# Performance work log

Hardware: AMD Instinct MI355X
Metric: run time of the kernel (lower is better)

The kernel has to match this reference:

```python
import jax, jax.numpy as jnp
import numpy as np

B, N, DIM, H, DH = 8, 1024, 512, 8, 64
INNER = H * DH  # 512
G = DH // 4     # SE(3) groups of size 4 per head


def setup_inputs() -> dict:
    key = jax.random.key(0)
    ks = jax.random.split(key, 6)
    x = jax.random.normal(ks[0], (B, N, DIM), jnp.float32)
    rotations = jax.random.normal(ks[1], (B, N, 3, 3), jnp.float32)
    translations = jax.random.normal(ks[2], (B, N, 3), jnp.float32)
    # JaxLinear init: trunc-normal std = 1/sqrt(fan_in), zero bias
    w_qkv = jax.random.normal(ks[3], (DIM, 3 * INNER), jnp.float32) * (1.0 / np.sqrt(DIM))
    b_qkv = jnp.zeros((3 * INNER,), jnp.float32)
    w_out = jax.random.normal(ks[4], (INNER, DIM), jnp.float32) * (1.0 / np.sqrt(INNER))
    b_out = jnp.zeros((DIM,), jnp.float32)
    return {"x": x, "rotations": rotations, "translations": translations,
            "w_qkv": w_qkv, "b_qkv": b_qkv, "w_out": w_out, "b_out": b_out}


def _apply_pose(P, t, transpose):
    # P: [B,N,4,4]; t: [B,H,N,DH] -> reshape to groups of 4 and rotate each group
    tg = t.reshape(B, H, N, G, 4)
    sub = 'bnji,bhncj->bhnci' if transpose else 'bnij,bhncj->bhnci'
    return jnp.einsum(sub, P, tg).reshape(B, H, N, DH)


def reference(x, rotations, translations, w_qkv, b_qkv, w_out, b_out):
    scale = DH ** -0.5
    qkv = x @ w_qkv + b_qkv                      # [B,N,3*INNER]
    q, k, v = jnp.split(qkv, 3, axis=-1)
    to_heads = lambda t: t.reshape(B, N, H, DH).transpose(0, 2, 1, 3)  # b n (h d) -> b h n d
    q, k, v = to_heads(q), to_heads(k), to_heads(v)

    # SE(3) pose matrices
    eye4 = jnp.eye(4, dtype=x.dtype)
    Rt = jnp.swapaxes(rotations, -1, -2)
    t_inv = -jnp.einsum('bnij,bnj->bni', Rt, translations)
    P_qinv = (jnp.broadcast_to(eye4, (B, N, 4, 4))
              .at[..., :3, :3].set(Rt)
              .at[..., :3, 3].set(t_inv))       # inverted query poses
    P_kv = (jnp.broadcast_to(eye4, (B, N, 4, 4))
            .at[..., :3, :3].set(rotations)
            .at[..., :3, 3].set(translations))  # key/value poses

    # per-token rotation of q/k/v (q uses P_qinv^T per original einsum)
    q = _apply_pose(P_qinv, q, transpose=True)
    k = _apply_pose(P_kv, k, transpose=False)
    v = _apply_pose(P_kv, v, transpose=False)   # v_transform=True

    attn = jax.nn.softmax(jnp.einsum('bhqd,bhkd->bhqk', q, k) * scale, axis=-1)
    out = jnp.einsum('bhqk,bhkd->bhqd', attn, v)
    out = _apply_pose(P_qinv, out, transpose=False)  # inverse transform on output

    out = out.transpose(0, 2, 1, 3).reshape(B, N, INNER)  # b h n d -> b n (h d)
    return out @ w_out + b_out
```

## Files before the change

kernel.cpp:

```cpp
#include <hip/hip_runtime.h>
#include <math.h>

#define BSZ   8
#define NSEQ  1024
#define DIM   512
#define NH    8
#define DH    64
#define INNER 512
#define NTOK  (BSZ*NSEQ)
#define QKVN  (3*INNER)

typedef __bf16 bf16x8 __attribute__((ext_vector_type(8)));
typedef float  f32x4  __attribute__((ext_vector_type(4)));

#define QSCL (0.125f * 1.44269504088896f)

static __device__ __forceinline__ ushort f2bf(float f) {
    union { float f; unsigned u; } v; v.f = f;
    unsigned r = (v.u + 0x7FFFu + ((v.u >> 16) & 1u)) >> 16;
    return (ushort)r;
}
static __device__ __forceinline__ float bf2f(ushort u) {
    union { unsigned u; float f; } v; v.u = ((unsigned)u) << 16;
    return v.f;
}
static __device__ __forceinline__ void split2(float x, ushort& h, ushort& l) {
    h = f2bf(x);
    l = f2bf(x - bf2f(h));
}
static __device__ __forceinline__ void async16(const void* g, void* l) {
    __builtin_amdgcn_global_load_lds(
        (const __attribute__((address_space(1))) unsigned int*)g,
        (__attribute__((address_space(3))) unsigned int*)l, 16, 0, 0);
}

__global__ __launch_bounds__(256) void split_cvt_kernel(
    const float* __restrict__ in, ushort* __restrict__ oh, ushort* __restrict__ ol)
{
    const int i = blockIdx.x * 256 + threadIdx.x;
    float4 v = ((const float4*)in)[i];
    ushort4 h, l;
    split2(v.x, h.x, l.x); split2(v.y, h.y, l.y);
    split2(v.z, h.z, l.z); split2(v.w, h.w, l.w);
    ((ushort4*)oh)[i] = h;
    ((ushort4*)ol)[i] = l;
}

__global__ __launch_bounds__(256) void tconv_kernel(
    const float* __restrict__ in, ushort* __restrict__ outh, int K, int F)
{
    __shared__ float tile[32][33];
    const int bx = blockIdx.x;
    const int by = blockIdx.y;
    const int lx = threadIdx.x & 31, ly = threadIdx.x >> 5;
#pragma unroll
    for (int u = 0; u < 4; u++) {
        const int k = by*32 + ly + u*8;
        tile[ly + u*8][lx] = in[(size_t)k*F + bx*32 + lx];
    }
    __syncthreads();
#pragma unroll
    for (int u = 0; u < 4; u++) {
        const int f = bx*32 + ly + u*8;
        outh[(size_t)f*K + by*32 + lx] = f2bf(tile[lx][ly + u*8]);
    }
}

__global__ __launch_bounds__(256) void qkv_gemm_split(
    const ushort* __restrict__ Agh, const ushort* __restrict__ Bgh,
    const ushort* __restrict__ Bgl,
    const float* __restrict__ bias, const float* __restrict__ rot,
    const float* __restrict__ trans,
    ushort* __restrict__ qb, ushort* __restrict__ kb, ushort* __restrict__ vt)
{
    extern __shared__ __align__(16) char smem[];

    const int tid  = threadIdx.x;
    const int lane = tid & 63;
    const int w    = tid >> 6;
    const int c    = lane & 15;
    const int quad = lane >> 4;
    const int wr   = w >> 1, wc = w & 1;
    const int tn   = blockIdx.x;
    const int tf   = blockIdx.y;

    f32x4 acc[4][4] = {};

    const ushort* wp = (w == 0) ? Agh : (w == 1) ? Bgh : Bgl;
    const ushort* wbase = wp + (size_t)((w == 0 ? tf : tn)*128 + c)*DIM + quad*8;
    const int lbase = w * 8192;

    auto stage = [&](int k0, int buf) {
        if (w < 3) {
#pragma unroll
            for (int g = 0; g < 8; g++)
                async16(wbase + (size_t)g*16*DIM + k0,
                        smem + buf*24576 + lbase + g*1024);
        }
    };

    stage(0, 0);

    for (int ch = 0; ch < 16; ch++) {
        const int cur = ch & 1, nxt = cur ^ 1;
        if (ch < 15) {
            stage((ch+1)*32, nxt);
            __asm__ volatile("s_waitcnt vmcnt(8)\n\ts_barrier" ::: "memory");
        } else {
            __asm__ volatile("s_waitcnt vmcnt(0)\n\ts_barrier" ::: "memory");
        }

        const char* B = smem + cur*24576;
        bf16x8 fa[4], fbh[4], fbl[4];
#pragma unroll
        for (int i = 0; i < 4; i++)
            fa[i] = *(const bf16x8*)(B + (wr*4 + i)*1024 + lane*16);
#pragma unroll
        for (int j = 0; j < 4; j++) {
            fbh[j] = *(const bf16x8*)(B +  8192 + (wc*4 + j)*1024 + lane*16);
            fbl[j] = *(const bf16x8*)(B + 16384 + (wc*4 + j)*1024 + lane*16);
        }
#pragma unroll
        for (int i = 0; i < 4; i++)
#pragma unroll
            for (int j = 0; j < 4; j++) {
                acc[i][j] = __builtin_amdgcn_mfma_f32_16x16x32_bf16(
                    fa[i], fbh[j], acc[i][j], 0, 0, 0);
                acc[i][j] = __builtin_amdgcn_mfma_f32_16x16x32_bf16(
                    fa[i], fbl[j], acc[i][j], 0, 0, 0);
            }
        __asm__ volatile("s_waitcnt lgkmcnt(0)\n\ts_barrier" ::: "memory");
    }

    const int sec = tf >> 2;

#pragma unroll
    for (int j = 0; j < 4; j++) {
        const int tc = tn*128 + wc*64 + j*16 + c;
        const int bb = tc >> 10, n = tc & 1023;
        const float* R = rot   + (size_t)(bb*NSEQ + n)*9;
        const float* T = trans + (size_t)(bb*NSEQ + n)*3;
        const float R0=R[0],R1=R[1],R2=R[2],R3=R[3],R4=R[4],R5=R[5],R6=R[6],R7=R[7],R8=R[8];
        const float T0=T[0],T1=T[1],T2=T[2];
        float ti0 = 0.f, ti1 = 0.f, ti2 = 0.f;
        if (sec == 0) {
            ti0 = -(R0*T0 + R3*T1 + R6*T2);
            ti1 = -(R1*T0 + R4*T1 + R7*T2);
            ti2 = -(R2*T0 + R5*T1 + R8*T2);
        }
#pragma unroll
        for (int i = 0; i < 4; i++) {
            const int fr = tf*128 + wr*64 + i*16 + quad*4;
            const int fl = fr & 511;
            const int h  = fl >> 6, d = fl & 63;
            float4 bv = *(const float4*)(bias + fr);
            const float g0 = acc[i][j][0] + bv.x;
            const float g1 = acc[i][j][1] + bv.y;
            const float g2 = acc[i][j][2] + bv.z;
            const float g3 = acc[i][j][3] + bv.w;
            if (sec == 0) {
                float o0 = (R0*g0 + R1*g1 + R2*g2) * QSCL;
                float o1 = (R3*g0 + R4*g1 + R5*g2) * QSCL;
                float o2 = (R6*g0 + R7*g1 + R8*g2) * QSCL;
                float o3 = (ti0*g0 + ti1*g1 + ti2*g2 + g3) * QSCL;
                ushort4 ov = { f2bf(o0), f2bf(o1), f2bf(o2), f2bf(o3) };
                *(ushort4*)(qb + ((size_t)((bb*NH + h)*NSEQ + n))*DH + d) = ov;
            } else {
                float o0 = R0*g0 + R1*g1 + R2*g2 + T0*g3;
                float o1 = R3*g0 + R4*g1 + R5*g2 + T1*g3;
                float o2 = R6*g0 + R7*g1 + R8*g2 + T2*g3;
                float o3 = g3;
                if (sec == 1) {
                    ushort4 ov = { f2bf(o0), f2bf(o1), f2bf(o2), f2bf(o3) };
                    *(ushort4*)(kb + ((size_t)((bb*NH + h)*NSEQ + n))*DH + d) = ov;
                } else {
                    ushort* vtb = vt + ((size_t)(bb*NH + h)*DH + d)*NSEQ + n;
                    vtb[0*NSEQ] = f2bf(o0);
                    vtb[1*NSEQ] = f2bf(o1);
                    vtb[2*NSEQ] = f2bf(o2);
                    vtb[3*NSEQ] = f2bf(o3);
                }
            }
        }
    }
}

__global__ __launch_bounds__(256) void attn_mfma_kernel(
    const ushort* __restrict__ qb, const ushort* __restrict__ kb,
    const ushort* __restrict__ vt, const float* __restrict__ rot,
    const float* __restrict__ trans, ushort* __restrict__ om)
{
    __shared__ __align__(16) char smem[51200];

    const int tid  = threadIdx.x;
    const int lane = tid & 63;
    const int w    = tid >> 6;
    const int c    = lane & 15;
    const int quad = lane >> 4;

    const int qt = blockIdx.x;
    const int bh = blockIdx.y;
    const int bb = bh >> 3, h = bh & 7;

    const ushort* Q = qb + (size_t)bh * NSEQ * DH;
    const ushort* K = kb + (size_t)bh * NSEQ * DH;
    const ushort* V = vt + (size_t)bh * DH * NSEQ;

    bf16x8 qf[2][2];
#pragma unroll
    for (int m = 0; m < 2; m++) {
        const ushort* qrow = Q + (size_t)(qt*128 + w*32 + m*16 + c)*DH + quad*8;
        qf[m][0] = *(const bf16x8*)(qrow);
        qf[m][1] = *(const bf16x8*)(qrow + 32);
    }

    f32x4 Oacc[2][4] = {};
    float lsum[2][4] = {};

    auto stage = [&](int kt, int buf) {
#pragma unroll
        for (int u = 0; u < 2; u++) {
            const int seg = w + u*4;
            const int nt = seg >> 1, hh = seg & 1;
            const ushort* g = K + (size_t)(kt*64 + nt*16 + c)*DH + hh*32 + quad*8;
            async16(g, smem + buf*16384 + seg*1024);
        }
#pragma unroll
        for (int u = 0; u < 2; u++) {
            const int s2 = w + u*4;
            const int nt = s2 >> 1, kc = s2 & 1;
            const ushort* g = V + (size_t)(nt*16 + c)*NSEQ + kt*64 + kc*32 + quad*8;
            async16(g, smem + buf*16384 + 8192 + s2*1024);
        }
    };

    stage(0, 0);

    for (int kt = 0; kt < 16; kt++) {
        const int cur = kt & 1, nxt = cur ^ 1;
        if (kt < 15) {
            stage(kt+1, nxt);
            __asm__ volatile("s_waitcnt vmcnt(4)\n\ts_barrier" ::: "memory");
        } else {
            __asm__ volatile("s_waitcnt vmcnt(0)\n\ts_barrier" ::: "memory");
        }

        const char* Kb = smem + cur*16384;
        const char* Vb = smem + cur*16384 + 8192;

        f32x4 s[2][4];
#pragma unroll
        for (int nt = 0; nt < 4; nt++) {
            bf16x8 k0 = *(const bf16x8*)(Kb + (nt*2+0)*1024 + lane*16);
            bf16x8 k1 = *(const bf16x8*)(Kb + (nt*2+1)*1024 + lane*16);
#pragma unroll
            for (int m = 0; m < 2; m++) {
                f32x4 a = {0.f, 0.f, 0.f, 0.f};
                a = __builtin_amdgcn_mfma_f32_16x16x32_bf16(qf[m][0], k0, a, 0, 0, 0);
                a = __builtin_amdgcn_mfma_f32_16x16x32_bf16(qf[m][1], k1, a, 0, 0, 0);
                s[m][nt] = a;
            }
        }

#pragma unroll
        for (int m = 0; m < 2; m++) {
            ushort (*Psw)[72] = (ushort (*)[72])(smem + 32768 + (w*2+m)*2304);
#pragma unroll
            for (int nt = 0; nt < 4; nt++)
#pragma unroll
                for (int r = 0; r < 4; r++) {
                    const float p = exp2f(s[m][nt][r]);
                    lsum[m][r] += p;
                    Psw[quad*4 + r][nt*16 + c] = (ushort)__builtin_bit_cast(
                        unsigned short, (__bf16)p);
                }
        }
        __asm__ volatile("s_waitcnt lgkmcnt(0)" ::: "memory");

#pragma unroll
        for (int kc = 0; kc < 2; kc++) {
            bf16x8 vfr[4];
#pragma unroll
            for (int nt = 0; nt < 4; nt++)
                vfr[nt] = *(const bf16x8*)(Vb + (nt*2+kc)*1024 + lane*16);
#pragma unroll
            for (int m = 0; m < 2; m++) {
                ushort (*Psw)[72] = (ushort (*)[72])(smem + 32768 + (w*2+m)*2304);
                bf16x8 a = *(const bf16x8*)&Psw[c][kc*32 + quad*8];
#pragma unroll
                for (int nt = 0; nt < 4; nt++)
                    Oacc[m][nt] = __builtin_amdgcn_mfma_f32_16x16x32_bf16(
                        a, vfr[nt], Oacc[m][nt], 0, 0, 0);
            }
        }
        __asm__ volatile("s_waitcnt lgkmcnt(0)\n\ts_barrier" ::: "memory");
    }

#pragma unroll
    for (int mk = 1; mk < 16; mk <<= 1)
#pragma unroll
        for (int m = 0; m < 2; m++)
#pragma unroll
            for (int r = 0; r < 4; r++)
                lsum[m][r] += __shfl_xor(lsum[m][r], mk);

    __syncthreads();
    float (*Osh)[68] = (float (*)[68])smem;
    {
        float inv[2][4];
#pragma unroll
        for (int m = 0; m < 2; m++)
#pragma unroll
            for (int r = 0; r < 4; r++) inv[m][r] = 1.f / lsum[m][r];
#pragma unroll
        for (int m = 0; m < 2; m++)
#pragma unroll
            for (int nt = 0; nt < 4; nt++)
#pragma unroll
                for (int r = 0; r < 4; r++)
                    Osh[w*32 + m*16 + quad*4 + r][nt*16 + c] =
                        Oacc[m][nt][r] * inv[m][r];
    }
    __syncthreads();

#pragma unroll
    for (int u = 0; u < 8; u++) {
        const int t   = tid + u*256;
        const int row = t >> 4;
        const int g   = t & 15;
        const int n   = qt*128 + row;
        const float o0 = Osh[row][g*4+0], o1 = Osh[row][g*4+1];
        const float o2 = Osh[row][g*4+2], o3 = Osh[row][g*4+3];
        const float* R = rot   + (size_t)(bb*NSEQ + n)*9;
        const float* T = trans + (size_t)(bb*NSEQ + n)*3;
        const float ti0 = -(R[0]*T[0] + R[3]*T[1] + R[6]*T[2]);
        const float ti1 = -(R[1]*T[0] + R[4]*T[1] + R[7]*T[2]);
        const float ti2 = -(R[2]*T[0] + R[5]*T[1] + R[8]*T[2]);
        const float p0 = R[0]*o0 + R[3]*o1 + R[6]*o2 + ti0*o3;
        const float p1 = R[1]*o0 + R[4]*o1 + R[7]*o2 + ti1*o3;
        const float p2 = R[2]*o0 + R[5]*o1 + R[8]*o2 + ti2*o3;
        const float p3 = o3;
        ushort4 hv = { f2bf(p0), f2bf(p1), f2bf(p2), f2bf(p3) };
        *(ushort4*)(om + (size_t)(bb*NSEQ + n)*INNER + h*DH + g*4) = hv;
    }
}

__global__ __launch_bounds__(256) void out_gemm_mfma(
    const ushort* __restrict__ Ag, const ushort* __restrict__ Bg,
    const float* __restrict__ bias, float* __restrict__ out)
{
    extern __shared__ __align__(16) char smem[];

    const int tid  = threadIdx.x;
    const int lane = tid & 63;
    const int w    = tid >> 6;
    const int c    = lane & 15;
    const int quad = lane >> 4;
    const int wr   = w >> 1, wc = w & 1;
    const int tn   = blockIdx.x;
    const int tf   = blockIdx.y;

    f32x4 acc[4][4] = {};

    const int part = w >> 1;
    const int g0   = (w & 1) * 4;
    const ushort* src = (part == 0) ? Ag : Bg;
    const ushort* wbase = src + (size_t)((part == 0 ? tf : tn)*128 + g0*16 + c)*INNER
                          + quad*8;

    auto stage = [&](int k0, int buf) {
#pragma unroll
        for (int g = 0; g < 4; g++)
            async16(wbase + (size_t)g*16*INNER + k0,
                    smem + buf*16384 + part*8192 + (g0 + g)*1024);
    };

    stage(0, 0);

    for (int ch = 0; ch < 16; ch++) {
        const int cur = ch & 1, nxt = cur ^ 1;
        if (ch < 15) {
            stage((ch+1)*32, nxt);
            __asm__ volatile("s_waitcnt vmcnt(4)\n\ts_barrier" ::: "memory");
        } else {
            __asm__ volatile("s_waitcnt vmcnt(0)\n\ts_barrier" ::: "memory");
        }

        const char* B = smem + cur*16384;
        bf16x8 fa[4], fb[4];
#pragma unroll
        for (int i = 0; i < 4; i++)
            fa[i] = *(const bf16x8*)(B + (wr*4 + i)*1024 + lane*16);
#pragma unroll
        for (int j = 0; j < 4; j++)
            fb[j] = *(const bf16x8*)(B + 8192 + (wc*4 + j)*1024 + lane*16);
#pragma unroll
        for (int i = 0; i < 4; i++)
#pragma unroll
            for (int j = 0; j < 4; j++)
                acc[i][j] = __builtin_amdgcn_mfma_f32_16x16x32_bf16(
                    fa[i], fb[j], acc[i][j], 0, 0, 0);
        __asm__ volatile("s_waitcnt lgkmcnt(0)\n\ts_barrier" ::: "memory");
    }

#pragma unroll
    for (int j = 0; j < 4; j++) {
        const int tc = tn*128 + wc*64 + j*16 + c;
#pragma unroll
        for (int i = 0; i < 4; i++) {
            const int fr = tf*128 + wr*64 + i*16 + quad*4;
            float4 bv = *(const float4*)(bias + fr);
            float4 ov = { acc[i][j][0] + bv.x, acc[i][j][1] + bv.y,
                          acc[i][j][2] + bv.z, acc[i][j][3] + bv.w };
            *(float4*)(out + (size_t)tc*DIM + fr) = ov;
        }
    }
}

extern "C" void kernel_launch(void* const* d_in, const int* in_sizes, int n_in,
                              void* d_out, int out_size, void* d_ws, size_t ws_size,
                              hipStream_t stream) {
    (void)in_sizes; (void)n_in; (void)out_size; (void)ws_size;
    const float* x     = (const float*)d_in[0];
    const float* rot   = (const float*)d_in[1];
    const float* trans = (const float*)d_in[2];
    const float* w_qkv = (const float*)d_in[3];
    const float* b_qkv = (const float*)d_in[4];
    const float* w_out = (const float*)d_in[5];
    const float* b_out = (const float*)d_in[6];
    float* out = (float*)d_out;

    const size_t HB = (size_t)BSZ*NH*NSEQ*DH;
    ushort* qb   = (ushort*)d_ws;
    ushort* kb   = qb   + HB;
    ushort* vt   = kb   + HB;
    ushort* woTh = vt   + HB;
    ushort* wqTh = woTh + (size_t)DIM*INNER;
    ushort* xh   = wqTh + (size_t)QKVN*DIM;
    ushort* xl   = xh   + HB;
    ushort* om   = xh;

    split_cvt_kernel<<<dim3(NTOK*DIM/1024), 256, 0, stream>>>(x, xh, xl);
    tconv_kernel<<<dim3(QKVN/32, DIM/32), 256, 0, stream>>>(w_qkv, wqTh, DIM, QKVN);
    tconv_kernel<<<dim3(DIM/32, INNER/32), 256, 0, stream>>>(w_out, woTh, INNER, DIM);

    qkv_gemm_split<<<dim3(NTOK/128, QKVN/128), 256, 49152, stream>>>(
        wqTh, xh, xl, b_qkv, rot, trans, qb, kb, vt);
    attn_mfma_kernel<<<dim3(NSEQ/128, BSZ*NH), 256, 0, stream>>>(
        qb, kb, vt, rot, trans, om);
    out_gemm_mfma<<<dim3(NTOK/128, DIM/128), 256, 32768, stream>>>(
        woTh, om, b_out, out);
}
```

Baseline: 178.8 us.

## Deepen LDS pipelines to triple/quad buffering and drop trailing barriers

Converts the double-buffered async global-to-LDS pipelines in the QKV GEMM, attention and output GEMM kernels into 3- and 4-stage rings. Prefetch is issued after the top-of-loop barrier, which lets the end-of-iteration lgkmcnt wait and barrier be removed. Dynamic shared memory grows, with raised attribute limits, to hide more global-load latency. The cost is more LDS per block, which can lower occupancy, and the ordering between LDS reads and buffer reuse now relies only on the single barrier per iteration.

```diff
diff --git a/kernel.cpp b/kernel.cpp
--- a/kernel.cpp
+++ b/kernel.cpp
@@ -14,6 +14,9 @@
 typedef float  f32x4  __attribute__((ext_vector_type(4)));
 
 #define QSCL (0.125f * 1.44269504088896f)
+
+#define ATTN_P_OFF 49152
+#define ATTN_LDS   67584
 
 static __device__ __forceinline__ ushort f2bf(float f) {
     union { float f; unsigned u; } v; v.f = f;
@@ -100,15 +103,16 @@
     };
 
     stage(0, 0);
+    stage(32, 1);
 
     for (int ch = 0; ch < 16; ch++) {
-        const int cur = ch & 1, nxt = cur ^ 1;
+        const int cur = ch % 3;
         if (ch < 15) {
-            stage((ch+1)*32, nxt);
             __asm__ volatile("s_waitcnt vmcnt(8)\n\ts_barrier" ::: "memory");
         } else {
             __asm__ volatile("s_waitcnt vmcnt(0)\n\ts_barrier" ::: "memory");
         }
+        if (ch < 14) stage((ch+2)*32, (ch+2) % 3);
 
         const char* B = smem + cur*24576;
         bf16x8 fa[4], fbh[4], fbl[4];
@@ -129,7 +133,6 @@
                 acc[i][j] = __builtin_amdgcn_mfma_f32_16x16x32_bf16(
                     fa[i], fbl[j], acc[i][j], 0, 0, 0);
             }
-        __asm__ volatile("s_waitcnt lgkmcnt(0)\n\ts_barrier" ::: "memory");
     }
 
     const int sec = tf >> 2;
@@ -190,7 +193,7 @@
     const ushort* __restrict__ vt, const float* __restrict__ rot,
     const float* __restrict__ trans, ushort* __restrict__ om)
 {
-    __shared__ __align__(16) char smem[51200];
+    extern __shared__ __align__(16) char smem[];
 
     const int tid  = threadIdx.x;
     const int lane = tid & 63;
@@ -235,15 +238,16 @@
     };
 
     stage(0, 0);
+    stage(1, 1);
 
     for (int kt = 0; kt < 16; kt++) {
-        const int cur = kt & 1, nxt = cur ^ 1;
+        const int cur = kt % 3;
         if (kt < 15) {
-            stage(kt+1, nxt);
             __asm__ volatile("s_waitcnt vmcnt(4)\n\ts_barrier" ::: "memory");
         } else {
             __asm__ volatile("s_waitcnt vmcnt(0)\n\ts_barrier" ::: "memory");
         }
+        if (kt < 14) stage(kt + 2, (kt + 2) % 3);
 
         const char* Kb = smem + cur*16384;
         const char* Vb = smem + cur*16384 + 8192;
@@ -264,7 +268,7 @@
 
 #pragma unroll
         for (int m = 0; m < 2; m++) {
-            ushort (*Psw)[72] = (ushort (*)[72])(smem + 32768 + (w*2+m)*2304);
+            ushort (*Psw)[72] = (ushort (*)[72])(smem + ATTN_P_OFF + (w*2+m)*2304);
 #pragma unroll
             for (int nt = 0; nt < 4; nt++)
 #pragma unroll
@@ -285,7 +289,7 @@
                 vfr[nt] = *(const bf16x8*)(Vb + (nt*2+kc)*1024 + lane*16);
 #pragma unroll
             for (int m = 0; m < 2; m++) {
-                ushort (*Psw)[72] = (ushort (*)[72])(smem + 32768 + (w*2+m)*2304);
+                ushort (*Psw)[72] = (ushort (*)[72])(smem + ATTN_P_OFF + (w*2+m)*2304);
                 bf16x8 a = *(const bf16x8*)&Psw[c][kc*32 + quad*8];
 #pragma unroll
                 for (int nt = 0; nt < 4; nt++)
@@ -293,7 +297,6 @@
                         a, vfr[nt], Oacc[m][nt], 0, 0, 0);
             }
         }
-        __asm__ volatile("s_waitcnt lgkmcnt(0)\n\ts_barrier" ::: "memory");
     }
 
 #pragma unroll
@@ -376,15 +379,19 @@
     };
 
     stage(0, 0);
+    stage(32, 1);
+    stage(64, 2);
 
     for (int ch = 0; ch < 16; ch++) {
-        const int cur = ch & 1, nxt = cur ^ 1;
-        if (ch < 15) {
-            stage((ch+1)*32, nxt);
+        const int cur = ch & 3;
+        if (ch < 14) {
+            __asm__ volatile("s_waitcnt vmcnt(8)\n\ts_barrier" ::: "memory");
+        } else if (ch == 14) {
             __asm__ volatile("s_waitcnt vmcnt(4)\n\ts_barrier" ::: "memory");
         } else {
             __asm__ volatile("s_waitcnt vmcnt(0)\n\ts_barrier" ::: "memory");
         }
+        if (ch < 13) stage((ch+3)*32, (ch+3) & 3);
 
         const char* B = smem + cur*16384;
         bf16x8 fa[4], fb[4];
@@ -400,7 +407,6 @@
             for (int j = 0; j < 4; j++)
                 acc[i][j] = __builtin_amdgcn_mfma_f32_16x16x32_bf16(
                     fa[i], fb[j], acc[i][j], 0, 0, 0);
-        __asm__ volatile("s_waitcnt lgkmcnt(0)\n\ts_barrier" ::: "memory");
     }
 
 #pragma unroll
@@ -440,14 +446,25 @@
     ushort* xl   = xh   + HB;
     ushort* om   = xh;
 
+    static int s_attr_done = 0;
+    if (!s_attr_done) {
+        (void)hipFuncSetAttribute((const void*)qkv_gemm_split,
+            hipFuncAttributeMaxDynamicSharedMemorySize, 73728);
+        (void)hipFuncSetAttribute((const void*)attn_mfma_kernel,
+            hipFuncAttributeMaxDynamicSharedMemorySize, ATTN_LDS);
+        (void)hipFuncSetAttribute((const void*)out_gemm_mfma,
+            hipFuncAttributeMaxDynamicSharedMemorySize, 65536);
+        s_attr_done = 1;
+    }
+
     split_cvt_kernel<<<dim3(NTOK*DIM/1024), 256, 0, stream>>>(x, xh, xl);
     tconv_kernel<<<dim3(QKVN/32, DIM/32), 256, 0, stream>>>(w_qkv, wqTh, DIM, QKVN);
     tconv_kernel<<<dim3(DIM/32, INNER/32), 256, 0, stream>>>(w_out, woTh, INNER, DIM);
 
-    qkv_gemm_split<<<dim3(NTOK/128, QKVN/128), 256, 49152, stream>>>(
+    qkv_gemm_split<<<dim3(NTOK/128, QKVN/128), 256, 73728, stream>>>(
         wqTh, xh, xl, b_qkv, rot, trans, qb, kb, vt);
-    attn_mfma_kernel<<<dim3(NSEQ/128, BSZ*NH), 256, 0, stream>>>(
+    attn_mfma_kernel<<<dim3(NSEQ/128, BSZ*NH), 256, ATTN_LDS, stream>>>(
         qb, kb, vt, rot, trans, om);
-    out_gemm_mfma<<<dim3(NTOK/128, DIM/128), 256, 32768, stream>>>(
+    out_gemm_mfma<<<dim3(NTOK/128, DIM/128), 256, 65536, stream>>>(
         woTh, om, b_out, out);
 }
```

After: 179.0 us. Within noise of the previous version (+0.1%).
